# Kernel optimization log

Measured on AMD Instinct MI355X. Metric: run time of the kernel, lower is better.

The kernel has to match this reference:

```python
import jax, jax.numpy as jnp
import numpy as np

N_NODES = 50000
N_EDGES = 800000
D_IN = 128
H1 = 128
H2 = 64
N_CLASSES = 4


def _sage_conv(x, src, dst, w_l, w_r, b, num_nodes):
    # PyG SAGEConv (aggr='mean'): out = lin_l(mean_{j->i} x_j) + lin_r(x_i)
    ones = jnp.ones((src.shape[0],), dtype=x.dtype)
    deg = jax.ops.segment_sum(ones, dst, num_segments=num_nodes)  # [N]
    agg = jax.ops.segment_sum(x[src], dst, num_segments=num_nodes)  # [N, d]
    agg = agg / jnp.maximum(deg, 1.0)[:, None]
    return agg @ w_l + b + x @ w_r


def setup_inputs() -> dict:
    key = jax.random.key(0)
    ks = jax.random.split(key, 12)
    x_content = jax.random.normal(ks[0], (N_NODES, D_IN), dtype=jnp.float32)
    edge_index = jax.random.randint(ks[1], (2, N_EDGES), 0, N_NODES, dtype=jnp.int32)
    edge_type = jax.random.randint(ks[2], (N_EDGES,), 0, 4, dtype=jnp.int32)
    s = 0.05
    params = {
        'w_l0': jax.random.normal(ks[3], (D_IN, H1), jnp.float32) * s,
        'w_r0': jax.random.normal(ks[4], (D_IN, H1), jnp.float32) * s,
        'b0': jnp.zeros((H1,), jnp.float32),
        'w_l1': jax.random.normal(ks[5], (H1, H1), jnp.float32) * s,
        'w_r1': jax.random.normal(ks[6], (H1, H1), jnp.float32) * s,
        'b1': jnp.zeros((H1,), jnp.float32),
        'w_l2': jax.random.normal(ks[7], (H1, H2), jnp.float32) * s,
        'w_r2': jax.random.normal(ks[8], (H1, H2), jnp.float32) * s,
        'b2': jnp.zeros((H2,), jnp.float32),
        'w_out': jax.random.normal(ks[9], (H2, N_CLASSES), jnp.float32) * s,
        'b_out': jnp.zeros((N_CLASSES,), jnp.float32),
    }
    return {'x_content': x_content, 'edge_index': edge_index, 'edge_type': edge_type, **params}


def reference(x_content, edge_index, edge_type,
              w_l0, w_r0, b0, w_l1, w_r1, b1, w_l2, w_r2, b2, w_out, b_out):
    # eval mode: dropout is identity
    src, dst = edge_index[0], edge_index[1]
    n = x_content.shape[0]
    x = x_content
    for (wl, wr, b) in ((w_l0, w_r0, b0), (w_l1, w_r1, b1), (w_l2, w_r2, b2)):
        x = _sage_conv(x, src, dst, wl, wr, b, n)
        x = jax.nn.relu(x)
    return x @ w_out + b_out
```

## Files before the change

kernel.cpp:

```cpp
#include <hip/hip_runtime.h>
#include <hip/hip_fp16.h>

#define D 128

constexpr int RSH = 14;
constexpr int RSZ = 1 << RSH;
constexpr int NRANGE = 4;
constexpr int CSH = 15;
constexpr int CSZ = 1 << CSH;

using short8 = __attribute__((ext_vector_type(8))) short;
using f32x4 = __attribute__((ext_vector_type(4))) float;

__device__ inline void splitf(float v, unsigned short& h, unsigned short& l) {
    unsigned b = __float_as_uint(v);
    h = (unsigned short)(b >> 16);
    float fh = __uint_as_float(b & 0xffff0000u);
    float r = v - fh;
    l = (unsigned short)(__float_as_uint(r) >> 16);
}

struct WSplitArgs {
    const float* src[6];
    unsigned short* dh[6];
    unsigned short* dl[6];
    int n[6];
};

__global__ __launch_bounds__(256) void split_w(WSplitArgs a) {
    int m = blockIdx.y;
    int N = a.n[m];
    int e = blockIdx.x * 256 + threadIdx.x;
    if (e >= 128 * N) return;
    int sh = (N == 128) ? 7 : 6;
    int k = e >> sh;
    int n = e & (N - 1);
    float v = a.src[m][e];
    unsigned short h, l;
    splitf(v, h, l);
    a.dh[m][n * 128 + k] = h;
    a.dl[m][n * 128 + k] = l;
}

__global__ __launch_bounds__(1024) void hist_gemm_x(
    const int* __restrict__ dst, unsigned* __restrict__ hist,
    unsigned short* __restrict__ rank, int n_edges, int nchunk, int nhist,
    const float* __restrict__ X,
    const unsigned short* __restrict__ W1h, const unsigned short* __restrict__ W1l,
    const unsigned short* __restrict__ W2h, const unsigned short* __restrict__ W2l,
    const float* __restrict__ bias, __half* __restrict__ P, float* __restrict__ Q, int M) {
    __shared__ __align__(16) char smem[2 * 16 * 65 * 16];

    const int b = blockIdx.x;
    const int tid = threadIdx.x;

    if (b < nhist) {
        unsigned* lh = (unsigned*)smem;
        int r = b & (NRANGE - 1), c = b >> 2;
        for (int i = tid; i < RSZ / 2; i += 1024) lh[i] = 0;
        __syncthreads();
        int e0 = c << CSH, e1 = min(n_edges, e0 + CSZ);
        for (int e = e0 + tid; e < e1; e += 1024) {
            int d = dst[e];
            if ((d >> RSH) == r) {
                int ii = d & (RSZ - 1);
                unsigned sh = (ii & 1) * 16;
                unsigned old = atomicAdd(&lh[ii >> 1], 1u << sh);
                rank[e] = (unsigned short)((old >> sh) & 0xffffu);
            }
        }
        __syncthreads();
        unsigned* gh = hist + (size_t)(r * nchunk + c) * (RSZ / 2);
        for (int i = tid; i < RSZ / 2; i += 1024) gh[i] = lh[i];
        return;
    }

    short8(*As)[16 * 65] = (short8(*)[16 * 65])smem;
    const int wave = tid >> 6;
    const int lane = tid & 63;
    const int l15 = lane & 15;
    const int q = lane >> 4;
    const int m0 = (b - nhist) * 64;

    {
        int row = tid >> 4, col16 = tid & 15;
        int gr = min(m0 + row, M - 1);
        const float4* xp = (const float4*)X + (size_t)gr * 32 + col16 * 2;
        float4 v0 = xp[0], v1 = xp[1];
        float fv[8] = {v0.x, v0.y, v0.z, v0.w, v1.x, v1.y, v1.z, v1.w};
        short8 h, l;
#pragma unroll
        for (int j = 0; j < 8; ++j) {
            unsigned short hh_, ll_;
            splitf(fv[j], hh_, ll_);
            h[j] = (short)hh_;
            l[j] = (short)ll_;
        }
        As[0][col16 * 65 + row] = h;
        As[1][col16 * 65 + row] = l;
    }
    __syncthreads();

    const int isQ = wave >> 3;
    const int colbase = (wave & 7) * 16;
    const unsigned short* Wh = isQ ? W2h : W1h;
    const unsigned short* Wl = isQ ? W2l : W1l;
    const float bv = isQ ? bias[colbase + l15] : 0.f;

    f32x4 acc[4] = {};

#pragma unroll 1
    for (int kt = 0; kt < 4; ++kt) {
        int c = colbase + l15;
        int woff = c * 128 + kt * 32 + q * 8;
        short8 Bh = *(const short8*)(Wh + woff);
        short8 Bl = *(const short8*)(Wl + woff);
#pragma unroll
        for (int mt = 0; mt < 4; ++mt) {
            int ai = (kt * 4 + q) * 65 + mt * 16 + l15;
            short8 Afh = As[0][ai];
            short8 Afl = As[1][ai];
            acc[mt] = __builtin_amdgcn_mfma_f32_16x16x32_bf16(Afh, Bh, acc[mt], 0, 0, 0);
            acc[mt] = __builtin_amdgcn_mfma_f32_16x16x32_bf16(Afh, Bl, acc[mt], 0, 0, 0);
            acc[mt] = __builtin_amdgcn_mfma_f32_16x16x32_bf16(Afl, Bh, acc[mt], 0, 0, 0);
        }
    }

#pragma unroll
    for (int mt = 0; mt < 4; ++mt) {
        int orow = m0 + mt * 16 + q * 4;
        int col = colbase + l15;
#pragma unroll
        for (int r = 0; r < 4; ++r) {
            int rr = orow + r;
            if (rr < M) {
                if (isQ) Q[(size_t)rr * 128 + col] = acc[mt][r] + bv;
                else P[(size_t)rr * 128 + col] = __float2half(acc[mt][r]);
            }
        }
    }
}

__global__ __launch_bounds__(256) void deg_sum_partials(
    const unsigned short* __restrict__ hist16, int* __restrict__ deg,
    int* __restrict__ partials, int n_nodes, int nchunk) {
    __shared__ int sd[256];
    int b = blockIdx.x, t = threadIdx.x;
    int i = b * 256 + t;
    int s = 0;
    if (i < n_nodes) {
        int r = i >> RSH, ii = i & (RSZ - 1);
        const unsigned short* hp = hist16 + (size_t)r * nchunk * RSZ + ii;
        for (int c = 0; c < nchunk; ++c) s += hp[(size_t)c * RSZ];
        deg[i] = s;
    }
    sd[t] = s;
    __syncthreads();
    for (int st = 128; st > 0; st >>= 1) {
        if (t < st) sd[t] += sd[t + st];
        __syncthreads();
    }
    if (t == 0) partials[b] = sd[0];
}

__global__ __launch_bounds__(256) void scan_fill(
    const int* __restrict__ deg, const int* __restrict__ partials,
    const unsigned short* __restrict__ hist16, int* __restrict__ row_ptr,
    float* __restrict__ inv_deg, int* __restrict__ base,
    int n_nodes, int nchunk, int nblk) {
    __shared__ int sp[256];
    __shared__ int sd[256];
    int b = blockIdx.x, t = threadIdx.x;

    sp[t] = (t < b && t < nblk) ? partials[t] : 0;
    __syncthreads();
    for (int st = 128; st > 0; st >>= 1) {
        if (t < st) sp[t] += sp[t + st];
        __syncthreads();
    }
    int pbase = sp[0];

    int i = b * 256 + t;
    int v = (i < n_nodes) ? deg[i] : 0;
    sd[t] = v;
    __syncthreads();
    for (int d = 1; d < 256; d <<= 1) {
        int x = (t >= d) ? sd[t - d] : 0;
        __syncthreads();
        sd[t] += x;
        __syncthreads();
    }
    int excl = sd[t] - v + pbase;
    if (i < n_nodes) {
        row_ptr[i] = excl;
        int dv = v > 1 ? v : 1;
        inv_deg[i] = 1.0f / (float)dv;
        if (i == n_nodes - 1) row_ptr[n_nodes] = excl + v;
        int r = i >> RSH, ii = i & (RSZ - 1);
        int bacc = excl;
        for (int c = 0; c < nchunk; ++c) {
            size_t idx = (size_t)(r * nchunk + c) * RSZ + ii;
            base[idx] = bacc;
            bacc += hist16[idx];
        }
    }
}

__global__ __launch_bounds__(256) void fill_edges(
    const int* __restrict__ src, const int* __restrict__ dst,
    const unsigned short* __restrict__ rank, const int* __restrict__ base,
    int* __restrict__ csr, int n_edges, int nchunk) {
    int e = blockIdx.x * 256 + threadIdx.x;
    if (e >= n_edges) return;
    int d = dst[e];
    int c = e >> CSH;
    int r = d >> RSH;
    int slot = base[(size_t)(r * nchunk + c) * RSZ + (d & (RSZ - 1))] + rank[e];
    csr[slot] = src[e];
}

template <int BN, int NT>
__global__ __launch_bounds__(256) void gemm_lds(
    const unsigned short* __restrict__ Ah, const unsigned short* __restrict__ Al,
    const unsigned short* __restrict__ W1h, const unsigned short* __restrict__ W1l,
    const unsigned short* __restrict__ W2h, const unsigned short* __restrict__ W2l,
    const float* __restrict__ bias, __half* __restrict__ P, float* __restrict__ Q, int M) {
    __shared__ short8 As[2][16 * 65];

    const int tid = threadIdx.x;
    const int wave = tid >> 6;
    const int lane = tid & 63;
    const int l15 = lane & 15;
    const int q = lane >> 4;
    const int m0 = blockIdx.x * 64;

#pragma unroll
    for (int it = 0; it < 8; ++it) {
        int s = it * 256 + tid;
        int arr = s >> 10;
        int sp = s & 1023;
        int row = sp >> 4, col16 = sp & 15;
        int gr = min(m0 + row, M - 1);
        const unsigned short* src = (arr ? Al : Ah) + (size_t)gr * 128 + col16 * 8;
        As[arr][col16 * 65 + row] = *(const short8*)src;
    }
    __syncthreads();

    const int isQ = wave >> 1;
    const int colbase = (wave & 1) * (NT * 16);
    const unsigned short* Wh = isQ ? W2h : W1h;
    const unsigned short* Wl = isQ ? W2l : W1l;

    float bvs[NT];
#pragma unroll
    for (int nt = 0; nt < NT; ++nt) bvs[nt] = isQ ? bias[colbase + nt * 16 + l15] : 0.f;

    f32x4 acc[4][NT] = {};

#pragma unroll 1
    for (int kt = 0; kt < 4; ++kt) {
        short8 Bh[NT], Bl[NT];
#pragma unroll
        for (int nt = 0; nt < NT; ++nt) {
            int c = colbase + nt * 16 + l15;
            int off = c * 128 + kt * 32 + q * 8;
            Bh[nt] = *(const short8*)(Wh + off);
            Bl[nt] = *(const short8*)(Wl + off);
        }
#pragma unroll
        for (int mt = 0; mt < 4; ++mt) {
            int ai = (kt * 4 + q) * 65 + mt * 16 + l15;
            short8 Afh = As[0][ai];
            short8 Afl = As[1][ai];
#pragma unroll
            for (int nt = 0; nt < NT; ++nt) {
                acc[mt][nt] = __builtin_amdgcn_mfma_f32_16x16x32_bf16(Afh, Bh[nt], acc[mt][nt], 0, 0, 0);
                acc[mt][nt] = __builtin_amdgcn_mfma_f32_16x16x32_bf16(Afh, Bl[nt], acc[mt][nt], 0, 0, 0);
                acc[mt][nt] = __builtin_amdgcn_mfma_f32_16x16x32_bf16(Afl, Bh[nt], acc[mt][nt], 0, 0, 0);
            }
        }
    }

#pragma unroll
    for (int mt = 0; mt < 4; ++mt) {
        int orow = m0 + mt * 16 + q * 4;
#pragma unroll
        for (int nt = 0; nt < NT; ++nt) {
            int col = colbase + nt * 16 + l15;
#pragma unroll
            for (int r = 0; r < 4; ++r) {
                int rr = orow + r;
                if (rr < M) {
                    if (isQ) Q[(size_t)rr * BN + col] = acc[mt][nt][r] + bvs[nt];
                    else P[(size_t)rr * BN + col] = __float2half(acc[mt][nt][r]);
                }
            }
        }
    }
}

__global__ __launch_bounds__(256) void agg_fused128(
    const __half* __restrict__ P, const float* __restrict__ Q,
    const int* __restrict__ row_ptr, const int* __restrict__ csr,
    const float* __restrict__ inv_deg, unsigned short* __restrict__ Hh,
    unsigned short* __restrict__ Hl, int n_nodes) {
    int node = (blockIdx.x * blockDim.x + threadIdx.x) >> 6;
    int lane = threadIdx.x & 63;
    if (node >= n_nodes) return;
    int beg = row_ptr[node], end = row_ptr[node + 1];
    const int g = lane >> 4;
    const int l = lane & 15;
    float a[2][8] = {};
    int e = beg;
    bool have = (e + 8 <= end);
    int i0 = 0, i1 = 0;
    if (have) { i0 = csr[e + g]; i1 = csr[e + 4 + g]; }
    while (have) {
        int en = e + 8;
        bool hn = (en + 8 <= end);
        int n0 = 0, n1 = 0;
        if (hn) { n0 = csr[en + g]; n1 = csr[en + 4 + g]; }
        int ss[2] = {i0, i1};
#pragma unroll
        for (int j = 0; j < 2; ++j) {
            uint4 raw = *(const uint4*)(P + (size_t)ss[j] * 128 + l * 8);
            float2 f01 = __half22float2(*reinterpret_cast<__half2*>(&raw.x));
            float2 f23 = __half22float2(*reinterpret_cast<__half2*>(&raw.y));
            float2 f45 = __half22float2(*reinterpret_cast<__half2*>(&raw.z));
            float2 f67 = __half22float2(*reinterpret_cast<__half2*>(&raw.w));
            a[j][0] += f01.x; a[j][1] += f01.y; a[j][2] += f23.x; a[j][3] += f23.y;
            a[j][4] += f45.x; a[j][5] += f45.y; a[j][6] += f67.x; a[j][7] += f67.y;
        }
        e = en; i0 = n0; i1 = n1; have = hn;
    }
    for (; e < end; e += 4) {
        int idx = e + g;
        if (idx < end) {
            int s = csr[idx];
            uint4 raw = *(const uint4*)(P + (size_t)s * 128 + l * 8);
            float2 f01 = __half22float2(*reinterpret_cast<__half2*>(&raw.x));
            float2 f23 = __half22float2(*reinterpret_cast<__half2*>(&raw.y));
            float2 f45 = __half22float2(*reinterpret_cast<__half2*>(&raw.z));
            float2 f67 = __half22float2(*reinterpret_cast<__half2*>(&raw.w));
            a[0][0] += f01.x; a[0][1] += f01.y; a[0][2] += f23.x; a[0][3] += f23.y;
            a[0][4] += f45.x; a[0][5] += f45.y; a[0][6] += f67.x; a[0][7] += f67.y;
        }
    }
    float s[8];
#pragma unroll
    for (int k = 0; k < 8; ++k) {
        s[k] = a[0][k] + a[1][k];
        s[k] += __shfl_xor(s[k], 16);
        s[k] += __shfl_xor(s[k], 32);
    }
    if (lane < 16) {
        float w = inv_deg[node];
        const float4* Q4 = (const float4*)Q;
        float4 q0 = Q4[(size_t)node * 32 + 2 * l];
        float4 q1 = Q4[(size_t)node * 32 + 2 * l + 1];
        float h0 = fmaxf(fmaf(s[0], w, q0.x), 0.f);
        float h1 = fmaxf(fmaf(s[1], w, q0.y), 0.f);
        float h2 = fmaxf(fmaf(s[2], w, q0.z), 0.f);
        float h3 = fmaxf(fmaf(s[3], w, q0.w), 0.f);
        float h4 = fmaxf(fmaf(s[4], w, q1.x), 0.f);
        float h5 = fmaxf(fmaf(s[5], w, q1.y), 0.f);
        float h6 = fmaxf(fmaf(s[6], w, q1.z), 0.f);
        float h7 = fmaxf(fmaf(s[7], w, q1.w), 0.f);
        ushort4 hv0, lv0, hv1, lv1;
        splitf(h0, hv0.x, lv0.x);
        splitf(h1, hv0.y, lv0.y);
        splitf(h2, hv0.z, lv0.z);
        splitf(h3, hv0.w, lv0.w);
        splitf(h4, hv1.x, lv1.x);
        splitf(h5, hv1.y, lv1.y);
        splitf(h6, hv1.z, lv1.z);
        splitf(h7, hv1.w, lv1.w);
        ((ushort4*)Hh)[(size_t)node * 32 + 2 * l] = hv0;
        ((ushort4*)Hh)[(size_t)node * 32 + 2 * l + 1] = hv1;
        ((ushort4*)Hl)[(size_t)node * 32 + 2 * l] = lv0;
        ((ushort4*)Hl)[(size_t)node * 32 + 2 * l + 1] = lv1;
    }
}

__global__ __launch_bounds__(256) void agg64_head(
    const __half* __restrict__ P, const float* __restrict__ Q,
    const int* __restrict__ row_ptr, const int* __restrict__ csr,
    const float* __restrict__ inv_deg, const float* __restrict__ Wo,
    const float* __restrict__ bo, float* __restrict__ out, int n_nodes) {
    int node = (blockIdx.x * blockDim.x + threadIdx.x) >> 6;
    int lane = threadIdx.x & 63;
    if (node >= n_nodes) return;
    int beg = row_ptr[node], end = row_ptr[node + 1];
    const int quarter = lane >> 4;
    const int l = lane & 15;
    float a[2][4] = {};
    int e = beg;
    bool have = (e + 8 <= end);
    int i0 = 0, i1 = 0;
    if (have) { i0 = csr[e + quarter]; i1 = csr[e + 4 + quarter]; }
    while (have) {
        int en = e + 8;
        bool hn = (en + 8 <= end);
        int n0 = 0, n1 = 0;
        if (hn) { n0 = csr[en + quarter]; n1 = csr[en + 4 + quarter]; }
        int ss[2] = {i0, i1};
#pragma unroll
        for (int j = 0; j < 2; ++j) {
            uint2 raw = *(const uint2*)(P + (size_t)ss[j] * 64 + l * 4);
            float2 f01 = __half22float2(*reinterpret_cast<__half2*>(&raw.x));
            float2 f23 = __half22float2(*reinterpret_cast<__half2*>(&raw.y));
            a[j][0] += f01.x; a[j][1] += f01.y; a[j][2] += f23.x; a[j][3] += f23.y;
        }
        e = en; i0 = n0; i1 = n1; have = hn;
    }
    for (; e < end; e += 4) {
        int idx = e + quarter;
        if (idx < end) {
            int s = csr[idx];
            uint2 raw = *(const uint2*)(P + (size_t)s * 64 + l * 4);
            float2 f01 = __half22float2(*reinterpret_cast<__half2*>(&raw.x));
            float2 f23 = __half22float2(*reinterpret_cast<__half2*>(&raw.y));
            a[0][0] += f01.x; a[0][1] += f01.y; a[0][2] += f23.x; a[0][3] += f23.y;
        }
    }
    float s0 = a[0][0] + a[1][0];
    float s1 = a[0][1] + a[1][1];
    float s2 = a[0][2] + a[1][2];
    float s3 = a[0][3] + a[1][3];
    s0 += __shfl_xor(s0, 16); s0 += __shfl_xor(s0, 32);
    s1 += __shfl_xor(s1, 16); s1 += __shfl_xor(s1, 32);
    s2 += __shfl_xor(s2, 16); s2 += __shfl_xor(s2, 32);
    s3 += __shfl_xor(s3, 16); s3 += __shfl_xor(s3, 32);
    if (lane < 16) {
        float w = inv_deg[node];
        float4 qv = ((const float4*)Q)[(size_t)node * 16 + l];
        float h0 = fmaxf(fmaf(s0, w, qv.x), 0.f);
        float h1 = fmaxf(fmaf(s1, w, qv.y), 0.f);
        float h2 = fmaxf(fmaf(s2, w, qv.z), 0.f);
        float h3 = fmaxf(fmaf(s3, w, qv.w), 0.f);
        const float4* Wo4 = (const float4*)Wo;
        float4 w0 = Wo4[4 * l + 0], w1 = Wo4[4 * l + 1], w2 = Wo4[4 * l + 2], w3 = Wo4[4 * l + 3];
        float c0 = h0 * w0.x + h1 * w1.x + h2 * w2.x + h3 * w3.x;
        float c1 = h0 * w0.y + h1 * w1.y + h2 * w2.y + h3 * w3.y;
        float c2 = h0 * w0.z + h1 * w1.z + h2 * w2.z + h3 * w3.z;
        float c3 = h0 * w0.w + h1 * w1.w + h2 * w2.w + h3 * w3.w;
#pragma unroll
        for (int m = 8; m > 0; m >>= 1) {
            c0 += __shfl_xor(c0, m);
            c1 += __shfl_xor(c1, m);
            c2 += __shfl_xor(c2, m);
            c3 += __shfl_xor(c3, m);
        }
        if (l == 0) {
            float4 r;
            r.x = c0 + bo[0];
            r.y = c1 + bo[1];
            r.z = c2 + bo[2];
            r.w = c3 + bo[3];
            ((float4*)out)[node] = r;
        }
    }
}

extern "C" void kernel_launch(void* const* d_in, const int* in_sizes, int n_in,
                              void* d_out, int out_size, void* d_ws, size_t ws_size,
                              hipStream_t stream) {
    const float* x = (const float*)d_in[0];
    const int* ei = (const int*)d_in[1];
    const float* wl0 = (const float*)d_in[3];
    const float* wr0 = (const float*)d_in[4];
    const float* b0 = (const float*)d_in[5];
    const float* wl1 = (const float*)d_in[6];
    const float* wr1 = (const float*)d_in[7];
    const float* b1 = (const float*)d_in[8];
    const float* wl2 = (const float*)d_in[9];
    const float* wr2 = (const float*)d_in[10];
    const float* b2 = (const float*)d_in[11];
    const float* wo = (const float*)d_in[12];
    const float* bo = (const float*)d_in[13];

    const int n_nodes = in_sizes[0] / D;
    const int n_edges = in_sizes[1] / 2;
    const int* srcp = ei;
    const int* dstp = ei + n_edges;

    char* ws = (char*)d_ws;
    size_t off = 0;
    auto carve = [&](size_t bytes) -> void* {
        void* p = ws + off;
        off = (off + bytes + 255) & ~(size_t)255;
        return p;
    };
    int* deg = (int*)carve((size_t)n_nodes * 4);
    int* row_ptr = (int*)carve((size_t)(n_nodes + 1) * 4);
    int* partials = (int*)carve(256 * 4);
    float* inv_deg = (float*)carve((size_t)n_nodes * 4);
    unsigned short* rankb = (unsigned short*)carve((size_t)n_edges * 2);
    int* csr = (int*)carve((size_t)n_edges * 4);
    __half* Pbuf = (__half*)carve((size_t)n_nodes * D * 2);
    float* Qbuf = (float*)carve((size_t)n_nodes * D * 4);
    unsigned short* hh = (unsigned short*)carve((size_t)n_nodes * D * 2);
    unsigned short* hl = (unsigned short*)carve((size_t)n_nodes * D * 2);
    unsigned short* wt = (unsigned short*)carve((size_t)(4 * 128 * 128 + 2 * 64 * 128) * 2 * 2);
    unsigned short* wl0h = wt;
    unsigned short* wl0l = wl0h + 128 * 128;
    unsigned short* wr0h = wl0l + 128 * 128;
    unsigned short* wr0l = wr0h + 128 * 128;
    unsigned short* wl1h = wr0l + 128 * 128;
    unsigned short* wl1l = wl1h + 128 * 128;
    unsigned short* wr1h = wl1l + 128 * 128;
    unsigned short* wr1l = wr1h + 128 * 128;
    unsigned short* wl2h = wr1l + 128 * 128;
    unsigned short* wl2l = wl2h + 64 * 128;
    unsigned short* wr2h = wl2l + 64 * 128;
    unsigned short* wr2l = wr2h + 64 * 128;

    const int nchunk = (n_edges + CSZ - 1) >> CSH;
    unsigned* hist = (unsigned*)carve((size_t)NRANGE * nchunk * (RSZ / 2) * 4);
    unsigned short* hist16 = (unsigned short*)hist;
    int* basep = (int*)carve((size_t)NRANGE * nchunk * RSZ * 4);

    const int nblk = (n_nodes + 255) / 256;
    const int nhist = NRANGE * nchunk;
    const int gemm_blocks = (n_nodes + 63) / 64;
    const int agg_blocks = (n_nodes * 64 + 255) / 256;

    WSplitArgs wa;
    wa.src[0] = wl0; wa.dh[0] = wl0h; wa.dl[0] = wl0l; wa.n[0] = 128;
    wa.src[1] = wr0; wa.dh[1] = wr0h; wa.dl[1] = wr0l; wa.n[1] = 128;
    wa.src[2] = wl1; wa.dh[2] = wl1h; wa.dl[2] = wl1l; wa.n[2] = 128;
    wa.src[3] = wr1; wa.dh[3] = wr1h; wa.dl[3] = wr1l; wa.n[3] = 128;
    wa.src[4] = wl2; wa.dh[4] = wl2h; wa.dl[4] = wl2l; wa.n[4] = 64;
    wa.src[5] = wr2; wa.dh[5] = wr2h; wa.dl[5] = wr2l; wa.n[5] = 64;

    split_w<<<dim3(64, 6), 256, 0, stream>>>(wa);
    hist_gemm_x<<<nhist + gemm_blocks, 1024, 0, stream>>>(
        dstp, hist, rankb, n_edges, nchunk, nhist,
        x, wl0h, wl0l, wr0h, wr0l, b0, Pbuf, Qbuf, n_nodes);
    deg_sum_partials<<<nblk, 256, 0, stream>>>(hist16, deg, partials, n_nodes, nchunk);
    scan_fill<<<nblk, 256, 0, stream>>>(deg, partials, hist16, row_ptr, inv_deg, basep,
                                        n_nodes, nchunk, nblk);
    fill_edges<<<(n_edges + 255) / 256, 256, 0, stream>>>(srcp, dstp, rankb, basep, csr,
                                                          n_edges, nchunk);
    agg_fused128<<<agg_blocks, 256, 0, stream>>>(Pbuf, Qbuf, row_ptr, csr, inv_deg, hh, hl, n_nodes);
    gemm_lds<128, 4><<<gemm_blocks, 256, 0, stream>>>(
        hh, hl, wl1h, wl1l, wr1h, wr1l, b1, Pbuf, Qbuf, n_nodes);
    agg_fused128<<<agg_blocks, 256, 0, stream>>>(Pbuf, Qbuf, row_ptr, csr, inv_deg, hh, hl, n_nodes);
    gemm_lds<64, 2><<<gemm_blocks, 256, 0, stream>>>(
        hh, hl, wl2h, wl2l, wr2h, wr2l, b2, Pbuf, Qbuf, n_nodes);
    agg64_head<<<agg_blocks, 256, 0, stream>>>(Pbuf, Qbuf, row_ptr, csr, inv_deg,
                                               wo, bo, (float*)d_out, n_nodes);
}
```

Measured before the change: 289.8 us.

## Store P in column-blocked layout and aggregate each 32-column slice separately

The GEMMs that feed the 128-wide aggregations now write P as four contiguous slabs of 32 half columns per node. The aggregation kernel becomes a four-pass launch (grid.y = pass) in which each wave gathers only a 64-byte slice per neighbour for 8 neighbours at a time. Each slab covers about 3.2 MB, so it is meant to stay cache-resident and make the random gathers cheaper. In exchange the csr indices are re-read four times, the number of waves is four times larger, and the scattered 2-byte P stores may coalesce worse.

```diff
diff --git a/kernel.cpp b/kernel.cpp
--- a/kernel.cpp
+++ b/kernel.cpp
@@ -126,16 +126,17 @@
         }
     }
 
+    const int col = colbase + l15;
+    const int q4 = col >> 5, cw = col & 31;
 #pragma unroll
     for (int mt = 0; mt < 4; ++mt) {
         int orow = m0 + mt * 16 + q * 4;
-        int col = colbase + l15;
 #pragma unroll
         for (int r = 0; r < 4; ++r) {
             int rr = orow + r;
             if (rr < M) {
                 if (isQ) Q[(size_t)rr * 128 + col] = acc[mt][r] + bv;
-                else P[(size_t)rr * 128 + col] = __float2half(acc[mt][r]);
+                else P[(size_t)q4 * M * 32 + (size_t)rr * 32 + cw] = __float2half(acc[mt][r]);
             }
         }
     }
@@ -219,7 +220,7 @@
     csr[slot] = src[e];
 }
 
-template <int BN, int NT>
+template <int BN, int NT, bool BLOCKP>
 __global__ __launch_bounds__(256) void gemm_lds(
     const unsigned short* __restrict__ Ah, const unsigned short* __restrict__ Al,
     const unsigned short* __restrict__ W1h, const unsigned short* __restrict__ W1l,
@@ -291,94 +292,72 @@
             for (int r = 0; r < 4; ++r) {
                 int rr = orow + r;
                 if (rr < M) {
-                    if (isQ) Q[(size_t)rr * BN + col] = acc[mt][nt][r] + bvs[nt];
-                    else P[(size_t)rr * BN + col] = __float2half(acc[mt][nt][r]);
+                    if (isQ) {
+                        Q[(size_t)rr * BN + col] = acc[mt][nt][r] + bvs[nt];
+                    } else if constexpr (BLOCKP) {
+                        int q4 = col >> 5, cw = col & 31;
+                        P[(size_t)q4 * M * 32 + (size_t)rr * 32 + cw] = __float2half(acc[mt][nt][r]);
+                    } else {
+                        P[(size_t)rr * BN + col] = __float2half(acc[mt][nt][r]);
+                    }
                 }
             }
         }
     }
 }
 
-__global__ __launch_bounds__(256) void agg_fused128(
-    const __half* __restrict__ P, const float* __restrict__ Q,
+__global__ __launch_bounds__(256) void agg128_pass(
+    const __half* __restrict__ Pb, const float* __restrict__ Q,
     const int* __restrict__ row_ptr, const int* __restrict__ csr,
     const float* __restrict__ inv_deg, unsigned short* __restrict__ Hh,
     unsigned short* __restrict__ Hl, int n_nodes) {
-    int node = (blockIdx.x * blockDim.x + threadIdx.x) >> 6;
+    int node = blockIdx.x * 4 + (threadIdx.x >> 6);
+    int pass = blockIdx.y;
     int lane = threadIdx.x & 63;
     if (node >= n_nodes) return;
     int beg = row_ptr[node], end = row_ptr[node + 1];
-    const int g = lane >> 4;
-    const int l = lane & 15;
-    float a[2][8] = {};
+    const int g = lane >> 3;
+    const int l8 = lane & 7;
+    const __half* Pp = Pb + (size_t)pass * n_nodes * 32;
+    float a0 = 0.f, a1 = 0.f, a2 = 0.f, a3 = 0.f;
     int e = beg;
     bool have = (e + 8 <= end);
-    int i0 = 0, i1 = 0;
-    if (have) { i0 = csr[e + g]; i1 = csr[e + 4 + g]; }
+    int idx = have ? csr[e + g] : 0;
     while (have) {
         int en = e + 8;
         bool hn = (en + 8 <= end);
-        int n0 = 0, n1 = 0;
-        if (hn) { n0 = csr[en + g]; n1 = csr[en + 4 + g]; }
-        int ss[2] = {i0, i1};
-#pragma unroll
-        for (int j = 0; j < 2; ++j) {
-            uint4 raw = *(const uint4*)(P + (size_t)ss[j] * 128 + l * 8);
-            float2 f01 = __half22float2(*reinterpret_cast<__half2*>(&raw.x));
-            float2 f23 = __half22float2(*reinterpret_cast<__half2*>(&raw.y));
-            float2 f45 = __half22float2(*reinterpret_cast<__half2*>(&raw.z));
-            float2 f67 = __half22float2(*reinterpret_cast<__half2*>(&raw.w));
-            a[j][0] += f01.x; a[j][1] += f01.y; a[j][2] += f23.x; a[j][3] += f23.y;
-            a[j][4] += f45.x; a[j][5] += f45.y; a[j][6] += f67.x; a[j][7] += f67.y;
-        }
-        e = en; i0 = n0; i1 = n1; have = hn;
-    }
-    for (; e < end; e += 4) {
-        int idx = e + g;
-        if (idx < end) {
-            int s = csr[idx];
-            uint4 raw = *(const uint4*)(P + (size_t)s * 128 + l * 8);
-            float2 f01 = __half22float2(*reinterpret_cast<__half2*>(&raw.x));
-            float2 f23 = __half22float2(*reinterpret_cast<__half2*>(&raw.y));
-            float2 f45 = __half22float2(*reinterpret_cast<__half2*>(&raw.z));
-            float2 f67 = __half22float2(*reinterpret_cast<__half2*>(&raw.w));
-            a[0][0] += f01.x; a[0][1] += f01.y; a[0][2] += f23.x; a[0][3] += f23.y;
-            a[0][4] += f45.x; a[0][5] += f45.y; a[0][6] += f67.x; a[0][7] += f67.y;
-        }
-    }
-    float s[8];
-#pragma unroll
-    for (int k = 0; k < 8; ++k) {
-        s[k] = a[0][k] + a[1][k];
-        s[k] += __shfl_xor(s[k], 16);
-        s[k] += __shfl_xor(s[k], 32);
-    }
-    if (lane < 16) {
+        int nidx = hn ? csr[en + g] : 0;
+        uint2 raw = *(const uint2*)(Pp + (size_t)idx * 32 + l8 * 4);
+        float2 f01 = __half22float2(*reinterpret_cast<__half2*>(&raw.x));
+        float2 f23 = __half22float2(*reinterpret_cast<__half2*>(&raw.y));
+        a0 += f01.x; a1 += f01.y; a2 += f23.x; a3 += f23.y;
+        e = en; idx = nidx; have = hn;
+    }
+    if (e + g < end) {
+        int s = csr[e + g];
+        uint2 raw = *(const uint2*)(Pp + (size_t)s * 32 + l8 * 4);
+        float2 f01 = __half22float2(*reinterpret_cast<__half2*>(&raw.x));
+        float2 f23 = __half22float2(*reinterpret_cast<__half2*>(&raw.y));
+        a0 += f01.x; a1 += f01.y; a2 += f23.x; a3 += f23.y;
+    }
+    a0 += __shfl_xor(a0, 8); a0 += __shfl_xor(a0, 16); a0 += __shfl_xor(a0, 32);
+    a1 += __shfl_xor(a1, 8); a1 += __shfl_xor(a1, 16); a1 += __shfl_xor(a1, 32);
+    a2 += __shfl_xor(a2, 8); a2 += __shfl_xor(a2, 16); a2 += __shfl_xor(a2, 32);
+    a3 += __shfl_xor(a3, 8); a3 += __shfl_xor(a3, 16); a3 += __shfl_xor(a3, 32);
+    if (lane < 8) {
         float w = inv_deg[node];
-        const float4* Q4 = (const float4*)Q;
-        float4 q0 = Q4[(size_t)node * 32 + 2 * l];
-        float4 q1 = Q4[(size_t)node * 32 + 2 * l + 1];
-        float h0 = fmaxf(fmaf(s[0], w, q0.x), 0.f);
-        float h1 = fmaxf(fmaf(s[1], w, q0.y), 0.f);
-        float h2 = fmaxf(fmaf(s[2], w, q0.z), 0.f);
-        float h3 = fmaxf(fmaf(s[3], w, q0.w), 0.f);
-        float h4 = fmaxf(fmaf(s[4], w, q1.x), 0.f);
-        float h5 = fmaxf(fmaf(s[5], w, q1.y), 0.f);
-        float h6 = fmaxf(fmaf(s[6], w, q1.z), 0.f);
-        float h7 = fmaxf(fmaf(s[7], w, q1.w), 0.f);
-        ushort4 hv0, lv0, hv1, lv1;
-        splitf(h0, hv0.x, lv0.x);
-        splitf(h1, hv0.y, lv0.y);
-        splitf(h2, hv0.z, lv0.z);
-        splitf(h3, hv0.w, lv0.w);
-        splitf(h4, hv1.x, lv1.x);
-        splitf(h5, hv1.y, lv1.y);
-        splitf(h6, hv1.z, lv1.z);
-        splitf(h7, hv1.w, lv1.w);
-        ((ushort4*)Hh)[(size_t)node * 32 + 2 * l] = hv0;
-        ((ushort4*)Hh)[(size_t)node * 32 + 2 * l + 1] = hv1;
-        ((ushort4*)Hl)[(size_t)node * 32 + 2 * l] = lv0;
-        ((ushort4*)Hl)[(size_t)node * 32 + 2 * l + 1] = lv1;
+        float4 qv = *(const float4*)(Q + (size_t)node * 128 + pass * 32 + l8 * 4);
+        float h0 = fmaxf(fmaf(a0, w, qv.x), 0.f);
+        float h1 = fmaxf(fmaf(a1, w, qv.y), 0.f);
+        float h2 = fmaxf(fmaf(a2, w, qv.z), 0.f);
+        float h3 = fmaxf(fmaf(a3, w, qv.w), 0.f);
+        ushort4 hv, lv;
+        splitf(h0, hv.x, lv.x);
+        splitf(h1, hv.y, lv.y);
+        splitf(h2, hv.z, lv.z);
+        splitf(h3, hv.w, lv.w);
+        *(ushort4*)(Hh + (size_t)node * 128 + pass * 32 + l8 * 4) = hv;
+        *(ushort4*)(Hl + (size_t)node * 128 + pass * 32 + l8 * 4) = lv;
     }
 }
 
@@ -524,6 +503,7 @@
     const int nhist = NRANGE * nchunk;
     const int gemm_blocks = (n_nodes + 63) / 64;
     const int agg_blocks = (n_nodes * 64 + 255) / 256;
+    const int agg4_blocks = (n_nodes + 3) / 4;
 
     WSplitArgs wa;
     wa.src[0] = wl0; wa.dh[0] = wl0h; wa.dl[0] = wl0l; wa.n[0] = 128;
@@ -542,11 +522,13 @@
                                         n_nodes, nchunk, nblk);
     fill_edges<<<(n_edges + 255) / 256, 256, 0, stream>>>(srcp, dstp, rankb, basep, csr,
                                                           n_edges, nchunk);
-    agg_fused128<<<agg_blocks, 256, 0, stream>>>(Pbuf, Qbuf, row_ptr, csr, inv_deg, hh, hl, n_nodes);
-    gemm_lds<128, 4><<<gemm_blocks, 256, 0, stream>>>(
+    agg128_pass<<<dim3(agg4_blocks, 4), 256, 0, stream>>>(
+        Pbuf, Qbuf, row_ptr, csr, inv_deg, hh, hl, n_nodes);
+    gemm_lds<128, 4, true><<<gemm_blocks, 256, 0, stream>>>(
         hh, hl, wl1h, wl1l, wr1h, wr1l, b1, Pbuf, Qbuf, n_nodes);
-    agg_fused128<<<agg_blocks, 256, 0, stream>>>(Pbuf, Qbuf, row_ptr, csr, inv_deg, hh, hl, n_nodes);
-    gemm_lds<64, 2><<<gemm_blocks, 256, 0, stream>>>(
+    agg128_pass<<<dim3(agg4_blocks, 4), 256, 0, stream>>>(
+        Pbuf, Qbuf, row_ptr, csr, inv_deg, hh, hl, n_nodes);
+    gemm_lds<64, 2, false><<<gemm_blocks, 256, 0, stream>>>(
         hh, hl, wl2h, wl2l, wr2h, wr2l, b2, Pbuf, Qbuf, n_nodes);
     agg64_head<<<agg_blocks, 256, 0, stream>>>(Pbuf, Qbuf, row_ptr, csr, inv_deg,
                                                wo, bo, (float*)d_out, n_nodes);
```

After: 369.0 us. 1.27x slower.
